# Kernel tuning notes

Hardware: AMD Instinct MI355X
Metric: run time of the kernel (lower is better)

Reference implementation:

```python
import jax, jax.numpy as jnp
import numpy as np

N_NODES = 100000
HIDDEN = 128
N_EDGES = 2000000
OUT_DIM = 1


def setup_inputs() -> dict:
    key = jax.random.key(0)
    k1, k2, k3, k4 = jax.random.split(key, 4)
    x_src = jax.random.normal(k1, (N_NODES, HIDDEN), dtype=jnp.float32)
    x_dst = jax.random.normal(k2, (N_NODES, HIDDEN), dtype=jnp.float32)
    edge_label_index = jax.random.randint(k3, (2, N_EDGES), 0, N_NODES, dtype=jnp.int64)
    # nn.Linear(2*hidden, out) params (Kaiming-uniform-ish init scale)
    bound = 1.0 / np.sqrt(2 * HIDDEN)
    weight = jax.random.uniform(k4, (OUT_DIM, 2 * HIDDEN), minval=-bound, maxval=bound, dtype=jnp.float32)
    bias = jnp.zeros((OUT_DIM,), dtype=jnp.float32)
    return {"x_src": x_src, "x_dst": x_dst, "edge_label_index": edge_label_index,
            "weight": weight, "bias": bias}


def reference(x_src, x_dst, edge_label_index, weight, bias):
    # Gather endpoint embeddings: [E, H] each
    h_src = x_src[edge_label_index[0]]
    h_dst = x_dst[edge_label_index[1]]
    # Split the linear over the two halves to avoid materializing the [E, 2H] concat
    w_src, w_dst = weight[:, :HIDDEN], weight[:, HIDDEN:]  # [O, H] each
    out = h_src @ w_src.T + h_dst @ w_dst.T + bias  # [E, O]
    return out
```

## Files before the change

kernel.cpp:

```cpp
#include <hip/hip_runtime.h>

#define HIDDEN  128
#define N_NODES 100000
#define N_EDGES 2000000
#define NBLK    1024
#define NTHR    256
#define NCTR    64
#define NGO     8
#define CTR_STRIDE 32

typedef float f32x4 __attribute__((ext_vector_type(4)));
typedef int   i32x4 __attribute__((ext_vector_type(4)));

__global__ __launch_bounds__(NTHR) void fused_edge_decoder(
    const float* __restrict__ x_src,
    const float* __restrict__ x_dst,
    const int*   __restrict__ idx,
    const float* __restrict__ w,
    const float* __restrict__ bias,
    float* __restrict__ out,
    float* __restrict__ s_tab,
    float* __restrict__ d_tab,
    int*   __restrict__ cnt,
    int*   __restrict__ go)
{
    const int tid      = blockIdx.x * NTHR + threadIdx.x;
    const int nthreads = NBLK * NTHR;
    const int lane     = tid & 15;

    const f32x4* wv = reinterpret_cast<const f32x4*>(w);
    const f32x4 ws0 = wv[lane];
    const f32x4 ws1 = wv[lane + 16];
    const f32x4 wd0 = wv[lane + 32];
    const f32x4 wd1 = wv[lane + 48];

    const int group   = tid >> 4;
    const int ngroups = nthreads >> 4;

    #pragma unroll 2
    for (int node = group; node < N_NODES; node += ngroups) {
        const f32x4* xs = reinterpret_cast<const f32x4*>(x_src + (size_t)node * HIDDEN);
        const f32x4* xd = reinterpret_cast<const f32x4*>(x_dst + (size_t)node * HIDDEN);
        const f32x4 a0 = xs[lane];
        const f32x4 a1 = xs[lane + 16];
        const f32x4 b0 = xd[lane];
        const f32x4 b1 = xd[lane + 16];

        float ss = a0.x*ws0.x + a0.y*ws0.y + a0.z*ws0.z + a0.w*ws0.w
                 + a1.x*ws1.x + a1.y*ws1.y + a1.z*ws1.z + a1.w*ws1.w;
        float dd = b0.x*wd0.x + b0.y*wd0.y + b0.z*wd0.z + b0.w*wd0.w
                 + b1.x*wd1.x + b1.y*wd1.y + b1.z*wd1.z + b1.w*wd1.w;

        #pragma unroll
        for (int off = 8; off; off >>= 1) {
            ss += __shfl_xor(ss, off);
            dd += __shfl_xor(dd, off);
        }
        if (lane == 0) {
            __hip_atomic_store(&s_tab[node], ss, __ATOMIC_RELAXED, __HIP_MEMORY_SCOPE_AGENT);
            __hip_atomic_store(&d_tab[node], dd, __ATOMIC_RELAXED, __HIP_MEMORY_SCOPE_AGENT);
        }
    }

    __syncthreads();
    if (threadIdx.x == 0) {
        asm volatile("s_waitcnt vmcnt(0)" ::: "memory");
        __hip_atomic_fetch_add(&cnt[(blockIdx.x & (NCTR - 1)) * CTR_STRIDE],
                               1, __ATOMIC_RELAXED, __HIP_MEMORY_SCOPE_AGENT);
    }
    if (blockIdx.x == 0) {
        if (threadIdx.x < 64) {
            int sum = 0;
            do {
                __builtin_amdgcn_s_sleep(2);
                sum = __hip_atomic_load(&cnt[threadIdx.x * CTR_STRIDE],
                                        __ATOMIC_RELAXED, __HIP_MEMORY_SCOPE_AGENT);
                #pragma unroll
                for (int off = 32; off; off >>= 1) sum += __shfl_xor(sum, off);
            } while (sum < NBLK);
            if (threadIdx.x < NGO) {
                __hip_atomic_store(&go[threadIdx.x * CTR_STRIDE], 1,
                                   __ATOMIC_RELAXED, __HIP_MEMORY_SCOPE_AGENT);
            }
        }
    } else if (threadIdx.x == 0) {
        int* myg = &go[(blockIdx.x & (NGO - 1)) * CTR_STRIDE];
        while (__hip_atomic_load(myg, __ATOMIC_RELAXED, __HIP_MEMORY_SCOPE_AGENT) == 0) {
            __builtin_amdgcn_s_sleep(16);
        }
    }
    __syncthreads();

    const float bv = bias[0];
    const i32x4* ia = reinterpret_cast<const i32x4*>(idx);
    const i32x4* ib = reinterpret_cast<const i32x4*>(idx + N_EDGES);
    f32x4* ov = reinterpret_cast<f32x4*>(out);
    const int nt = N_EDGES / 8;

    if (tid < nt) {
        const int t = tid;
        const i32x4 a0 = __builtin_nontemporal_load(ia + 2 * t);
        const i32x4 a1 = __builtin_nontemporal_load(ia + 2 * t + 1);
        const i32x4 b0 = __builtin_nontemporal_load(ib + 2 * t);
        const i32x4 b1 = __builtin_nontemporal_load(ib + 2 * t + 1);

        f32x4 o0, o1;
        o0.x = s_tab[a0.x] + d_tab[b0.x] + bv;
        o0.y = s_tab[a0.y] + d_tab[b0.y] + bv;
        o0.z = s_tab[a0.z] + d_tab[b0.z] + bv;
        o0.w = s_tab[a0.w] + d_tab[b0.w] + bv;
        o1.x = s_tab[a1.x] + d_tab[b1.x] + bv;
        o1.y = s_tab[a1.y] + d_tab[b1.y] + bv;
        o1.z = s_tab[a1.z] + d_tab[b1.z] + bv;
        o1.w = s_tab[a1.w] + d_tab[b1.w] + bv;

        __builtin_nontemporal_store(o0, ov + 2 * t);
        __builtin_nontemporal_store(o1, ov + 2 * t + 1);
    }
}

extern "C" void kernel_launch(void* const* d_in, const int* in_sizes, int n_in,
                              void* d_out, int out_size, void* d_ws, size_t ws_size,
                              hipStream_t stream) {
    const float* x_src = (const float*)d_in[0];
    const float* x_dst = (const float*)d_in[1];
    const int*   idx   = (const int*)d_in[2];
    const float* w     = (const float*)d_in[3];
    const float* bias  = (const float*)d_in[4];
    float* out = (float*)d_out;

    float* s_tab = (float*)d_ws;
    float* d_tab = s_tab + N_NODES;
    int*   cnt   = (int*)(d_tab + N_NODES);
    int*   go    = cnt + NCTR * CTR_STRIDE;

    hipMemsetAsync(cnt, 0, (NCTR + NGO) * CTR_STRIDE * sizeof(int), stream);

    fused_edge_decoder<<<NBLK, NTHR, 0, stream>>>(
        x_src, x_dst, idx, w, bias, out, s_tab, d_tab, cnt, go);
}
```

Baseline: 47.12 us.

## Prefetch edge indices before node phase and double grid to 2048 blocks

The edge-index loads now start at kernel entry, so their DRAM traffic overlaps with the per-node projection phase and the grid barrier instead of following them. The grid doubles to 2048 blocks so each thread handles one vector of 4 edges. The node-loop unroll pragma is dropped and the spin-wait sleep on the go flag is shortened. The custom grid barrier only works if all 2048 blocks are resident at once, so register pressure from the prefetched indices could cause a deadlock or cut occupancy.

```diff
diff --git a/kernel.cpp b/kernel.cpp
--- a/kernel.cpp
+++ b/kernel.cpp
@@ -3,7 +3,7 @@
 #define HIDDEN  128
 #define N_NODES 100000
 #define N_EDGES 2000000
-#define NBLK    1024
+#define NBLK    2048
 #define NTHR    256
 #define NCTR    64
 #define NGO     8
@@ -28,6 +28,13 @@
     const int nthreads = NBLK * NTHR;
     const int lane     = tid & 15;
 
+    const int nt = N_EDGES / 4;
+    i32x4 pa = {0, 0, 0, 0}, pb = {0, 0, 0, 0};
+    if (tid < nt) {
+        pa = __builtin_nontemporal_load(reinterpret_cast<const i32x4*>(idx) + tid);
+        pb = __builtin_nontemporal_load(reinterpret_cast<const i32x4*>(idx + N_EDGES) + tid);
+    }
+
     const f32x4* wv = reinterpret_cast<const f32x4*>(w);
     const f32x4 ws0 = wv[lane];
     const f32x4 ws1 = wv[lane + 16];
@@ -37,7 +44,6 @@
     const int group   = tid >> 4;
     const int ngroups = nthreads >> 4;
 
-    #pragma unroll 2
     for (int node = group; node < N_NODES; node += ngroups) {
         const f32x4* xs = reinterpret_cast<const f32x4*>(x_src + (size_t)node * HIDDEN);
         const f32x4* xd = reinterpret_cast<const f32x4*>(x_dst + (size_t)node * HIDDEN);
@@ -86,36 +92,19 @@
     } else if (threadIdx.x == 0) {
         int* myg = &go[(blockIdx.x & (NGO - 1)) * CTR_STRIDE];
         while (__hip_atomic_load(myg, __ATOMIC_RELAXED, __HIP_MEMORY_SCOPE_AGENT) == 0) {
-            __builtin_amdgcn_s_sleep(16);
+            __builtin_amdgcn_s_sleep(8);
         }
     }
     __syncthreads();
 
-    const float bv = bias[0];
-    const i32x4* ia = reinterpret_cast<const i32x4*>(idx);
-    const i32x4* ib = reinterpret_cast<const i32x4*>(idx + N_EDGES);
-    f32x4* ov = reinterpret_cast<f32x4*>(out);
-    const int nt = N_EDGES / 8;
-
     if (tid < nt) {
-        const int t = tid;
-        const i32x4 a0 = __builtin_nontemporal_load(ia + 2 * t);
-        const i32x4 a1 = __builtin_nontemporal_load(ia + 2 * t + 1);
-        const i32x4 b0 = __builtin_nontemporal_load(ib + 2 * t);
-        const i32x4 b1 = __builtin_nontemporal_load(ib + 2 * t + 1);
-
-        f32x4 o0, o1;
-        o0.x = s_tab[a0.x] + d_tab[b0.x] + bv;
-        o0.y = s_tab[a0.y] + d_tab[b0.y] + bv;
-        o0.z = s_tab[a0.z] + d_tab[b0.z] + bv;
-        o0.w = s_tab[a0.w] + d_tab[b0.w] + bv;
-        o1.x = s_tab[a1.x] + d_tab[b1.x] + bv;
-        o1.y = s_tab[a1.y] + d_tab[b1.y] + bv;
-        o1.z = s_tab[a1.z] + d_tab[b1.z] + bv;
-        o1.w = s_tab[a1.w] + d_tab[b1.w] + bv;
-
-        __builtin_nontemporal_store(o0, ov + 2 * t);
-        __builtin_nontemporal_store(o1, ov + 2 * t + 1);
+        const float bv = bias[0];
+        f32x4 o;
+        o.x = s_tab[pa.x] + d_tab[pb.x] + bv;
+        o.y = s_tab[pa.y] + d_tab[pb.y] + bv;
+        o.z = s_tab[pa.z] + d_tab[pb.z] + bv;
+        o.w = s_tab[pa.w] + d_tab[pb.w] + bv;
+        __builtin_nontemporal_store(o, reinterpret_cast<f32x4*>(out) + tid);
     }
 }
 
```

Result: faster. 45.88 us (-2.6%).
